# Kernel tuning notes

Measured on AMD Instinct MI355X. Metric: run time of the kernel, lower is better.

Reference implementation:

```python
import jax, jax.numpy as jnp
import numpy as np

B, S, F, D = 64, 129, 768, 4
MOM = 0.9
EPS = 1e-6


def setup_inputs() -> dict:
    key = jax.random.key(0)
    ks = jax.random.split(key, 8)
    x = jax.random.normal(ks[0], (B, S, F), dtype=jnp.float32)
    labels = jax.random.randint(ks[1], (B,), 0, 16, dtype=jnp.int32)
    domain = jax.random.randint(ks[2], (B,), 0, D, dtype=jnp.int32)
    lmda = jax.random.beta(ks[3], 0.1, 0.1, (B, 1, 1)).astype(jnp.float32)
    d_rand = jax.random.randint(ks[4], (B,), 1, D, dtype=jnp.int32)  # range(1, num_domains)
    mean_buf = (0.1 * jax.random.normal(ks[5], (D, F))).astype(jnp.float32)
    var_buf = jax.random.uniform(ks[6], (D, F), minval=0.5, maxval=1.5, dtype=jnp.float32)
    hg_noise = jax.random.normal(ks[7], (B, S, F), dtype=jnp.float32)
    return {"input": x, "lmda": lmda, "mean_buf": mean_buf, "var_buf": var_buf,
            "hg_noise": hg_noise, "labels": labels, "domain": domain, "d_rand": d_rand}


def reference(input, lmda, mean_buf, var_buf, hg_noise, labels, domain, d_rand):
    x = input  # [B,S,F]
    b, s, f = x.shape
    d = mean_buf.shape[0]

    # --- per-domain mean/var over dims [0,1] (unbiased), momentum buffer update ---
    tok = x.reshape(b * s, f)
    seg = jnp.repeat(domain, s)  # [B*S]
    cnt = jax.ops.segment_sum(jnp.ones((b * s,), x.dtype), seg, num_segments=d)  # tokens/domain
    s1 = jax.ops.segment_sum(tok, seg, num_segments=d)          # [D,F]
    s2 = jax.ops.segment_sum(tok * tok, seg, num_segments=d)    # [D,F]
    n = cnt[:, None]
    mu_d = s1 / jnp.maximum(n, 1.0)
    var_d = (s2 - n * mu_d * mu_d) / jnp.maximum(n - 1.0, 1.0)  # unbiased, matches torch.var
    present = (cnt > 0)[:, None]
    new_mean = jnp.where(present, MOM * mean_buf + (1.0 - MOM) * mu_d, mean_buf)
    new_var = jnp.where(present, MOM * var_buf + (1.0 - MOM) * var_d, var_buf)

    # --- instance renorm over token dim (unbiased var) + cross-domain restyle ---
    mu_i = x.mean(1, keepdims=True)
    v_i = x.var(1, keepdims=True, ddof=1)
    x_normed = (x - mu_i) * jax.lax.rsqrt(v_i + EPS)
    ds = (domain + d_rand) % d
    x_new = x_normed * jnp.sqrt(new_var[ds] + EPS)[:, None, :] + new_mean[ds][:, None, :]
    x_mix = lmda * x + (1.0 - lmda) * x_new

    # --- Gaussian hallucinated samples from own-domain stats ---
    hg = new_mean[domain][:, None, :] + jnp.sqrt(new_var[domain] + EPS)[:, None, :] * hg_noise

    # --- pairwise euclidean distance + hard example mining + soft-margin triplet loss ---
    xe = jnp.concatenate([x, x_mix, hg], axis=0).reshape(3 * b, s * f)  # [3B, S*F]
    ln = jnp.concatenate([labels, labels, -jnp.ones((b,), labels.dtype)])
    sq = jnp.sum(xe * xe, axis=1)
    d2 = sq[:, None] + sq[None, :] - 2.0 * (xe @ xe.T)
    dist = jnp.sqrt(jnp.clip(d2, 1e-12))
    pos = ln[:, None] == ln[None, :]
    big = jnp.asarray(1e30, dist.dtype)
    dist_ap = jnp.max(jnp.where(pos, dist, -big), axis=1)
    dist_an = jnp.min(jnp.where(pos, big, dist), axis=1)
    tri_hard_loss = jnp.mean(jax.nn.softplus(dist_ap - dist_an))  # SoftMarginLoss, y=1

    return x_mix, tri_hard_loss, new_mean, new_var
```

## Files before the change

### kernel.cpp

```cpp
#include <hip/hip_runtime.h>
#include <math.h>

#define B_ 64
#define S_ 129
#define F_ 768
#define N3 192
#define BF 49152
#define NCHUNK 1548
#define GMAIN 256
#define GSZ 36864
#define NSPLIT 8

#define WS_NM   0
#define WS_SV   3072
#define WS_C1   6144
#define WS_C0   55296
#define WS_HGM  104448
#define WS_HGS  153600
#define WS_S1   202752
#define WS_S2   251904
#define WS_GRAM 301056
#define WS_PART 337920
#define WS_S1P  WS_PART
#define WS_S2P  (WS_PART + NSPLIT * BF)

#define OUT_LOSS 6340608
#define OUT_NM   6340609
#define OUT_NV   6343681

typedef unsigned int uint;
using short8v = __attribute__((ext_vector_type(8))) short;
using float4v = __attribute__((ext_vector_type(4))) float;

__global__ void k_bf_stats(const float* __restrict__ x,
                           float* __restrict__ s1p, float* __restrict__ s2p) {
    int part = blockIdx.x / 48;
    int blk  = blockIdx.x % 48;
    int t4 = blk * 256 + threadIdx.x;
    int b = t4 / 192, f = (t4 - b * 192) * 4;
    int s0 = part * 16;
    int s1e = s0 + 16 + (part == 7 ? 1 : 0);
    const float* p = x + (size_t)b * S_ * F_ + f;
    float4 a1 = {0.f,0.f,0.f,0.f}, a2 = {0.f,0.f,0.f,0.f};
    for (int s = s0; s < s1e; ++s) {
        float4 v = *(const float4*)(p + s * F_);
        a1.x += v.x; a1.y += v.y; a1.z += v.z; a1.w += v.w;
        a2.x += v.x*v.x; a2.y += v.y*v.y; a2.z += v.z*v.z; a2.w += v.w*v.w;
    }
    *(float4*)(s1p + part * BF + b * F_ + f) = a1;
    *(float4*)(s2p + part * BF + b * F_ + f) = a2;
}

__global__ void k_sum(const float* __restrict__ s1p, const float* __restrict__ s2p,
                      float* __restrict__ s1, float* __restrict__ s2) {
    int j = (blockIdx.x * 256 + threadIdx.x) * 4;
    float4 a1 = {0.f,0.f,0.f,0.f}, a2 = {0.f,0.f,0.f,0.f};
#pragma unroll
    for (int p = 0; p < NSPLIT; ++p) {
        float4 v1 = *(const float4*)(s1p + p * BF + j);
        float4 v2 = *(const float4*)(s2p + p * BF + j);
        a1.x += v1.x; a1.y += v1.y; a1.z += v1.z; a1.w += v1.w;
        a2.x += v2.x; a2.y += v2.y; a2.z += v2.z; a2.w += v2.w;
    }
    *(float4*)(s1 + j) = a1;
    *(float4*)(s2 + j) = a2;
}

__global__ void k_dom(const float* __restrict__ s1, const float* __restrict__ s2,
                      const int* __restrict__ domain,
                      const float* __restrict__ mean_buf, const float* __restrict__ var_buf,
                      float* __restrict__ nm_tab, float* __restrict__ sv_tab,
                      float* __restrict__ out_nm, float* __restrict__ out_nv) {
    int idx = blockIdx.x * 256 + threadIdx.x;
    if (idx >= F_ * 4) return;
    int f = idx >> 2, d = idx & 3;
    float a1 = 0.f, a2 = 0.f, cntf = 0.f;
#pragma unroll 8
    for (int b = 0; b < B_; ++b) {
        float v1 = s1[b * F_ + f];
        float v2 = s2[b * F_ + f];
        bool mk = (domain[b] == d);
        a1 += mk ? v1 : 0.0f;
        a2 += mk ? v2 : 0.0f;
        cntf += mk ? 1.0f : 0.0f;
    }
    float nm, nv;
    if (cntf > 0.f) {
        float n = cntf * (float)S_;
        float mu = a1 / n;
        float var = (a2 - n * mu * mu) / fmaxf(n - 1.0f, 1.0f);
        nm = 0.9f * mean_buf[d * F_ + f] + 0.1f * mu;
        nv = 0.9f * var_buf[d * F_ + f] + 0.1f * var;
    } else {
        nm = mean_buf[d * F_ + f];
        nv = var_buf[d * F_ + f];
    }
    out_nm[d * F_ + f] = nm;
    out_nv[d * F_ + f] = nv;
    nm_tab[d * F_ + f] = nm;
    sv_tab[d * F_ + f] = sqrtf(nv + 1e-6f);
}

__global__ void k_coef(const float* __restrict__ s1, const float* __restrict__ s2,
                       const float* __restrict__ lmda,
                       const int* __restrict__ domain, const int* __restrict__ d_rand,
                       const float* __restrict__ nm_tab, const float* __restrict__ sv_tab,
                       float* __restrict__ c1, float* __restrict__ c0,
                       float* __restrict__ hgm, float* __restrict__ hgs,
                       float* __restrict__ gram, float* __restrict__ out_loss) {
    int t = blockIdx.x * 256 + threadIdx.x;
    if (blockIdx.x < 144) gram[blockIdx.x * 256 + threadIdx.x] = 0.0f;
    if (blockIdx.x == 144 && threadIdx.x == 0) out_loss[0] = 0.0f;
    int b = t / F_, f = t - b * F_;
    float mu = s1[t] * (1.0f / (float)S_);
    float v  = (s2[t] - (float)S_ * mu * mu) * (1.0f / (float)(S_ - 1));
    float r  = rsqrtf(v + 1e-6f);
    int dm = domain[b];
    int ds = (dm + d_rand[b]) & 3;
    float sv = sv_tab[ds * F_ + f];
    float nm = nm_tab[ds * F_ + f];
    float lam = lmda[b];
    float rs = r * sv;
    c1[t] = lam + (1.0f - lam) * rs;
    c0[t] = (1.0f - lam) * (nm - mu * rs);
    hgm[t] = nm_tab[dm * F_ + f];
    hgs[t] = sv_tab[dm * F_ + f];
}

__device__ __forceinline__ uint pack2(float a, float b) {
    uint ua = __float_as_uint(a);
    uint ub = __float_as_uint(b);
    uint ha = (ua + 0x7FFFu + ((ua >> 16) & 1u)) >> 16;
    uint hb = (ub + 0x7FFFu + ((ub >> 16) & 1u)) & 0xFFFF0000u;
    return hb | ha;
}

__device__ __forceinline__ void bf16_store8(char* lds, int row, int g,
                                            float4 v0, float4 v1) {
    uint4 H;
    H.x = pack2(v0.x, v0.y);
    H.y = pack2(v0.z, v0.w);
    H.z = pack2(v1.x, v1.y);
    H.w = pack2(v1.z, v1.w);
    *(uint4*)(lds + row * 128 + ((g ^ (row & 7)) << 4)) = H;
}

__device__ __forceinline__ float4 fma4(float4 a, float4 x, float4 b) {
    float4 r;
    r.x = fmaf(a.x, x.x, b.x); r.y = fmaf(a.y, x.y, b.y);
    r.z = fmaf(a.z, x.z, b.z); r.w = fmaf(a.w, x.w, b.w);
    return r;
}

template <bool EXCL>
__global__ __launch_bounds__(512, 2)
void k_main(const float* __restrict__ x, const float* __restrict__ hgn,
            const float* __restrict__ c1, const float* __restrict__ c0,
            const float* __restrict__ hgm, const float* __restrict__ hgs,
            float* __restrict__ xmix, float* part, int npart) {
    __shared__ __align__(16) char LDS[24576];
    float4v acc[6][3];
#pragma unroll
    for (int i = 0; i < 6; ++i)
#pragma unroll
        for (int j = 0; j < 3; ++j)
            acc[i][j] = (float4v){0.f, 0.f, 0.f, 0.f};

    int tid = threadIdx.x;
    int b = tid >> 3;
    int g = tid & 7;
    int w = tid >> 6;
    int wr = (w >> 2) * 96, wc = (w & 3) * 48;
    int lane = tid & 63, m = lane & 15, qd = lane >> 4;

    int q = blockIdx.x;
    size_t goff; int cb;
    {
        int s = q / 12, f0 = (q - s * 12) * 64;
        goff = ((size_t)b * S_ + s) * F_ + f0 + (g << 3);
        cb = b * F_ + f0 + (g << 3);
    }
    float4 X0 = ((const float4*)(x + goff))[0];
    float4 X1 = ((const float4*)(x + goff))[1];
    float4 N0 = ((const float4*)(hgn + goff))[0];
    float4 N1 = ((const float4*)(hgn + goff))[1];
    float4 C1a = ((const float4*)(c1 + cb))[0], C1b = ((const float4*)(c1 + cb))[1];
    float4 C0a = ((const float4*)(c0 + cb))[0], C0b = ((const float4*)(c0 + cb))[1];
    float4 HMa = ((const float4*)(hgm + cb))[0], HMb = ((const float4*)(hgm + cb))[1];
    float4 HSa = ((const float4*)(hgs + cb))[0], HSb = ((const float4*)(hgs + cb))[1];

    for (; q < NCHUNK; q += GMAIN) {
        float4 M0 = fma4(C1a, X0, C0a);
        float4 M1 = fma4(C1b, X1, C0b);
        ((float4*)(xmix + goff))[0] = M0;
        ((float4*)(xmix + goff))[1] = M1;
        float4 H0 = fma4(HSa, N0, HMa);
        float4 H1 = fma4(HSb, N1, HMb);

        bf16_store8(LDS, b, g, X0, X1);
        bf16_store8(LDS, 64 + b, g, M0, M1);
        bf16_store8(LDS, 128 + b, g, H0, H1);
        __syncthreads();

        int qn = q + GMAIN;
        if (qn < NCHUNK) {
            int s = qn / 12, f0 = (qn - s * 12) * 64;
            goff = ((size_t)b * S_ + s) * F_ + f0 + (g << 3);
            cb = b * F_ + f0 + (g << 3);
            X0 = ((const float4*)(x + goff))[0];
            X1 = ((const float4*)(x + goff))[1];
            N0 = ((const float4*)(hgn + goff))[0];
            N1 = ((const float4*)(hgn + goff))[1];
            C1a = ((const float4*)(c1 + cb))[0]; C1b = ((const float4*)(c1 + cb))[1];
            C0a = ((const float4*)(c0 + cb))[0]; C0b = ((const float4*)(c0 + cb))[1];
            HMa = ((const float4*)(hgm + cb))[0]; HMb = ((const float4*)(hgm + cb))[1];
            HSa = ((const float4*)(hgs + cb))[0]; HSb = ((const float4*)(hgs + cb))[1];
        }

#pragma unroll
        for (int t = 0; t < 2; ++t) {
            short8v A[6];
#pragma unroll
            for (int i = 0; i < 6; ++i) {
                int row = wr + i * 16 + m;
                int go = (((t << 2) + qd) ^ (row & 7)) << 4;
                A[i] = *(const short8v*)(LDS + row * 128 + go);
            }
#pragma unroll
            for (int j = 0; j < 3; ++j) {
                int row = wc + j * 16 + m;
                int go = (((t << 2) + qd) ^ (row & 7)) << 4;
                short8v Bv = *(const short8v*)(LDS + row * 128 + go);
#pragma unroll
                for (int i = 0; i < 6; ++i)
                    acc[i][j] = __builtin_amdgcn_mfma_f32_16x16x32_bf16(A[i], Bv, acc[i][j], 0, 0, 0);
            }
        }
        __syncthreads();
    }

    float* dst = part + (size_t)(blockIdx.x % npart) * GSZ;
#pragma unroll
    for (int i = 0; i < 6; ++i)
#pragma unroll
        for (int j = 0; j < 3; ++j) {
            int base = (wr + i * 16 + qd * 4) * N3 + wc + j * 16 + m;
#pragma unroll
            for (int r = 0; r < 4; ++r) {
                int o = base + r * N3;
                if (EXCL) dst[o] = acc[i][j][r];
                else atomicAdd(dst + o, acc[i][j][r]);
            }
        }
}

__global__ void k_red(const float* __restrict__ part, float* __restrict__ gram, int npart) {
    int g  = blockIdx.x / 36;
    int jb = blockIdx.x % 36;
    int j = (jb * 256 + threadIdx.x) * 4;
    int p0 = g * 32;
    int p1 = (p0 + 32 < npart) ? p0 + 32 : npart;
    float4 s = {0.f, 0.f, 0.f, 0.f};
    for (int p = p0; p < p1; ++p) {
        float4 v = *(const float4*)(part + (size_t)p * GSZ + j);
        s.x += v.x; s.y += v.y; s.z += v.z; s.w += v.w;
    }
    atomicAdd(gram + j,     s.x);
    atomicAdd(gram + j + 1, s.y);
    atomicAdd(gram + j + 2, s.z);
    atomicAdd(gram + j + 3, s.w);
}

__global__ void k_loss(const float* __restrict__ gram, const int* __restrict__ labels,
                       float* __restrict__ out_loss) {
    __shared__ float sq[N3];
    __shared__ int ln[N3];
    int i = blockIdx.x, lane = threadIdx.x;
    for (int k = lane; k < N3; k += 64) {
        sq[k] = gram[k * (N3 + 1)];
        ln[k] = (k < 128) ? labels[k & 63] : -1;
    }
    __syncthreads();
    int li = ln[i];
    float si = sq[i];
    float ap = -1e30f, an = 1e30f;
    for (int j = lane; j < N3; j += 64) {
        float d2 = si + sq[j] - 2.0f * gram[i * N3 + j];
        float dist = sqrtf(fmaxf(d2, 1e-12f));
        bool pos = (li == ln[j]);
        ap = pos ? fmaxf(ap, dist) : ap;
        an = pos ? an : fminf(an, dist);
    }
#pragma unroll
    for (int off = 32; off; off >>= 1) {
        ap = fmaxf(ap, __shfl_xor(ap, off));
        an = fminf(an, __shfl_xor(an, off));
    }
    if (lane == 0) {
        float xv = ap - an;
        float sp = fmaxf(xv, 0.0f) + log1pf(expf(-fabsf(xv)));
        atomicAdd(out_loss, sp * (1.0f / (float)N3));
    }
}

extern "C" void kernel_launch(void* const* d_in, const int* in_sizes, int n_in,
                              void* d_out, int out_size, void* d_ws, size_t ws_size,
                              hipStream_t stream) {
    const float* x        = (const float*)d_in[0];
    const float* lmda     = (const float*)d_in[1];
    const float* mean_buf = (const float*)d_in[2];
    const float* var_buf  = (const float*)d_in[3];
    const float* hgn      = (const float*)d_in[4];
    const int*   labels   = (const int*)d_in[5];
    const int*   domain   = (const int*)d_in[6];
    const int*   d_rand   = (const int*)d_in[7];
    float* out = (float*)d_out;
    float* ws  = (float*)d_ws;

    long avail = (long)(ws_size / 4) - WS_PART;
    int npart = (int)(avail / GSZ);
    if (npart < 1) npart = 1;
    if (npart > GMAIN) npart = GMAIN;
    bool excl = (npart == GMAIN);
    int ngroups = (npart + 31) / 32;

    k_bf_stats<<<dim3(48 * NSPLIT), dim3(256), 0, stream>>>(x, ws + WS_S1P, ws + WS_S2P);
    k_sum<<<dim3(48), dim3(256), 0, stream>>>(ws + WS_S1P, ws + WS_S2P,
                                              ws + WS_S1, ws + WS_S2);
    k_dom<<<dim3(12), dim3(256), 0, stream>>>(ws + WS_S1, ws + WS_S2, domain,
                                              mean_buf, var_buf,
                                              ws + WS_NM, ws + WS_SV,
                                              out + OUT_NM, out + OUT_NV);
    k_coef<<<dim3(192), dim3(256), 0, stream>>>(ws + WS_S1, ws + WS_S2, lmda,
                                                domain, d_rand,
                                                ws + WS_NM, ws + WS_SV,
                                                ws + WS_C1, ws + WS_C0,
                                                ws + WS_HGM, ws + WS_HGS,
                                                ws + WS_GRAM, out + OUT_LOSS);
    if (!excl) {
        hipMemsetAsync(ws + WS_PART, 0, (size_t)npart * GSZ * 4, stream);
    }
    if (excl) {
        k_main<true><<<dim3(GMAIN), dim3(512), 0, stream>>>(
            x, hgn, ws + WS_C1, ws + WS_C0, ws + WS_HGM, ws + WS_HGS,
            out, ws + WS_PART, npart);
    } else {
        k_main<false><<<dim3(GMAIN), dim3(512), 0, stream>>>(
            x, hgn, ws + WS_C1, ws + WS_C0, ws + WS_HGM, ws + WS_HGS,
            out, ws + WS_PART, npart);
    }
    k_red<<<dim3(ngroups * 36), dim3(256), 0, stream>>>(ws + WS_PART, ws + WS_GRAM, npart);
    k_loss<<<dim3(N3), dim3(64), 0, stream>>>(ws + WS_GRAM, labels, out + OUT_LOSS);
}
```

Baseline: 159.2 us.

## Double-buffer main Gram LDS, fuse stats reduction, replace atomic gram reduce

The main Gram kernel now alternates between two LDS buffers, which removes the trailing barrier in each chunk iteration at the cost of doubling shared memory per block. This may reduce occupancy under the 2-blocks launch bound. The per-sample stats pass is merged into a single kernel that reduces over the token dimension in LDS, dropping the separate partial-sum kernel and its global round trip. The partial Gram reduction becomes one non-atomic pass that writes the gram into a slot after the partials, so the gram zeroing in the coefficient kernel is removed and one fewer partial slot is available.

```diff
diff --git a/kernel.cpp b/kernel.cpp
--- a/kernel.cpp
+++ b/kernel.cpp
@@ -9,7 +9,6 @@
 #define NCHUNK 1548
 #define GMAIN 256
 #define GSZ 36864
-#define NSPLIT 8
 
 #define WS_NM   0
 #define WS_SV   3072
@@ -19,10 +18,7 @@
 #define WS_HGS  153600
 #define WS_S1   202752
 #define WS_S2   251904
-#define WS_GRAM 301056
 #define WS_PART 337920
-#define WS_S1P  WS_PART
-#define WS_S2P  (WS_PART + NSPLIT * BF)
 
 #define OUT_LOSS 6340608
 #define OUT_NM   6340609
@@ -32,38 +28,35 @@
 using short8v = __attribute__((ext_vector_type(8))) short;
 using float4v = __attribute__((ext_vector_type(4))) float;
 
-__global__ void k_bf_stats(const float* __restrict__ x,
-                           float* __restrict__ s1p, float* __restrict__ s2p) {
-    int part = blockIdx.x / 48;
-    int blk  = blockIdx.x % 48;
-    int t4 = blk * 256 + threadIdx.x;
-    int b = t4 / 192, f = (t4 - b * 192) * 4;
-    int s0 = part * 16;
-    int s1e = s0 + 16 + (part == 7 ? 1 : 0);
+__global__ void k_stats(const float* __restrict__ x,
+                        float* __restrict__ s1, float* __restrict__ s2) {
+    __shared__ float4 r1[256], r2[256];
+    int b = blockIdx.x / 3, fg = blockIdx.x % 3;
+    int c = threadIdx.x & 63, sp = threadIdx.x >> 6;
+    int f = fg * 256 + c * 4;
     const float* p = x + (size_t)b * S_ * F_ + f;
+    int s0 = sp * 32;
+    int se = s0 + 32 + (sp == 3 ? 1 : 0);
     float4 a1 = {0.f,0.f,0.f,0.f}, a2 = {0.f,0.f,0.f,0.f};
-    for (int s = s0; s < s1e; ++s) {
+#pragma unroll 4
+    for (int s = s0; s < se; ++s) {
         float4 v = *(const float4*)(p + s * F_);
         a1.x += v.x; a1.y += v.y; a1.z += v.z; a1.w += v.w;
         a2.x += v.x*v.x; a2.y += v.y*v.y; a2.z += v.z*v.z; a2.w += v.w*v.w;
     }
-    *(float4*)(s1p + part * BF + b * F_ + f) = a1;
-    *(float4*)(s2p + part * BF + b * F_ + f) = a2;
-}
-
-__global__ void k_sum(const float* __restrict__ s1p, const float* __restrict__ s2p,
-                      float* __restrict__ s1, float* __restrict__ s2) {
-    int j = (blockIdx.x * 256 + threadIdx.x) * 4;
-    float4 a1 = {0.f,0.f,0.f,0.f}, a2 = {0.f,0.f,0.f,0.f};
-#pragma unroll
-    for (int p = 0; p < NSPLIT; ++p) {
-        float4 v1 = *(const float4*)(s1p + p * BF + j);
-        float4 v2 = *(const float4*)(s2p + p * BF + j);
-        a1.x += v1.x; a1.y += v1.y; a1.z += v1.z; a1.w += v1.w;
-        a2.x += v2.x; a2.y += v2.y; a2.z += v2.z; a2.w += v2.w;
-    }
-    *(float4*)(s1 + j) = a1;
-    *(float4*)(s2 + j) = a2;
+    r1[threadIdx.x] = a1; r2[threadIdx.x] = a2;
+    __syncthreads();
+    if (sp == 0) {
+        float4 t1 = r1[c], t2 = r2[c];
+#pragma unroll
+        for (int k = 1; k < 4; ++k) {
+            float4 u1 = r1[k * 64 + c], u2 = r2[k * 64 + c];
+            t1.x += u1.x; t1.y += u1.y; t1.z += u1.z; t1.w += u1.w;
+            t2.x += u2.x; t2.y += u2.y; t2.z += u2.z; t2.w += u2.w;
+        }
+        *(float4*)(s1 + b * F_ + f) = t1;
+        *(float4*)(s2 + b * F_ + f) = t2;
+    }
 }
 
 __global__ void k_dom(const float* __restrict__ s1, const float* __restrict__ s2,
@@ -107,10 +100,9 @@
                        const float* __restrict__ nm_tab, const float* __restrict__ sv_tab,
                        float* __restrict__ c1, float* __restrict__ c0,
                        float* __restrict__ hgm, float* __restrict__ hgs,
-                       float* __restrict__ gram, float* __restrict__ out_loss) {
+                       float* __restrict__ out_loss) {
     int t = blockIdx.x * 256 + threadIdx.x;
-    if (blockIdx.x < 144) gram[blockIdx.x * 256 + threadIdx.x] = 0.0f;
-    if (blockIdx.x == 144 && threadIdx.x == 0) out_loss[0] = 0.0f;
+    if (blockIdx.x == 0 && threadIdx.x == 0) out_loss[0] = 0.0f;
     int b = t / F_, f = t - b * F_;
     float mu = s1[t] * (1.0f / (float)S_);
     float v  = (s2[t] - (float)S_ * mu * mu) * (1.0f / (float)(S_ - 1));
@@ -158,7 +150,7 @@
             const float* __restrict__ c1, const float* __restrict__ c0,
             const float* __restrict__ hgm, const float* __restrict__ hgs,
             float* __restrict__ xmix, float* part, int npart) {
-    __shared__ __align__(16) char LDS[24576];
+    __shared__ __align__(16) char LDS[49152];
     float4v acc[6][3];
 #pragma unroll
     for (int i = 0; i < 6; ++i)
@@ -189,7 +181,9 @@
     float4 HMa = ((const float4*)(hgm + cb))[0], HMb = ((const float4*)(hgm + cb))[1];
     float4 HSa = ((const float4*)(hgs + cb))[0], HSb = ((const float4*)(hgs + cb))[1];
 
+    int par = 0;
     for (; q < NCHUNK; q += GMAIN) {
+        char* buf = LDS + par * 24576;
         float4 M0 = fma4(C1a, X0, C0a);
         float4 M1 = fma4(C1b, X1, C0b);
         ((float4*)(xmix + goff))[0] = M0;
@@ -197,9 +191,9 @@
         float4 H0 = fma4(HSa, N0, HMa);
         float4 H1 = fma4(HSb, N1, HMb);
 
-        bf16_store8(LDS, b, g, X0, X1);
-        bf16_store8(LDS, 64 + b, g, M0, M1);
-        bf16_store8(LDS, 128 + b, g, H0, H1);
+        bf16_store8(buf, b, g, X0, X1);
+        bf16_store8(buf, 64 + b, g, M0, M1);
+        bf16_store8(buf, 128 + b, g, H0, H1);
         __syncthreads();
 
         int qn = q + GMAIN;
@@ -224,19 +218,19 @@
             for (int i = 0; i < 6; ++i) {
                 int row = wr + i * 16 + m;
                 int go = (((t << 2) + qd) ^ (row & 7)) << 4;
-                A[i] = *(const short8v*)(LDS + row * 128 + go);
+                A[i] = *(const short8v*)(buf + row * 128 + go);
             }
 #pragma unroll
             for (int j = 0; j < 3; ++j) {
                 int row = wc + j * 16 + m;
                 int go = (((t << 2) + qd) ^ (row & 7)) << 4;
-                short8v Bv = *(const short8v*)(LDS + row * 128 + go);
+                short8v Bv = *(const short8v*)(buf + row * 128 + go);
 #pragma unroll
                 for (int i = 0; i < 6; ++i)
                     acc[i][j] = __builtin_amdgcn_mfma_f32_16x16x32_bf16(A[i], Bv, acc[i][j], 0, 0, 0);
             }
         }
-        __syncthreads();
+        par ^= 1;
     }
 
     float* dst = part + (size_t)(blockIdx.x % npart) * GSZ;
@@ -255,20 +249,11 @@
 }
 
 __global__ void k_red(const float* __restrict__ part, float* __restrict__ gram, int npart) {
-    int g  = blockIdx.x / 36;
-    int jb = blockIdx.x % 36;
-    int j = (jb * 256 + threadIdx.x) * 4;
-    int p0 = g * 32;
-    int p1 = (p0 + 32 < npart) ? p0 + 32 : npart;
-    float4 s = {0.f, 0.f, 0.f, 0.f};
-    for (int p = p0; p < p1; ++p) {
-        float4 v = *(const float4*)(part + (size_t)p * GSZ + j);
-        s.x += v.x; s.y += v.y; s.z += v.z; s.w += v.w;
-    }
-    atomicAdd(gram + j,     s.x);
-    atomicAdd(gram + j + 1, s.y);
-    atomicAdd(gram + j + 2, s.z);
-    atomicAdd(gram + j + 3, s.w);
+    int j = blockIdx.x * 256 + threadIdx.x;
+    float s = 0.0f;
+#pragma unroll 8
+    for (int p = 0; p < npart; ++p) s += part[(size_t)p * GSZ + j];
+    gram[j] = s;
 }
 
 __global__ void k_loss(const float* __restrict__ gram, const int* __restrict__ labels,
@@ -318,15 +303,14 @@
     float* ws  = (float*)d_ws;
 
     long avail = (long)(ws_size / 4) - WS_PART;
-    int npart = (int)(avail / GSZ);
+    int npart = (int)(avail / GSZ) - 1;
     if (npart < 1) npart = 1;
     if (npart > GMAIN) npart = GMAIN;
     bool excl = (npart == GMAIN);
-    int ngroups = (npart + 31) / 32;
-
-    k_bf_stats<<<dim3(48 * NSPLIT), dim3(256), 0, stream>>>(x, ws + WS_S1P, ws + WS_S2P);
-    k_sum<<<dim3(48), dim3(256), 0, stream>>>(ws + WS_S1P, ws + WS_S2P,
-                                              ws + WS_S1, ws + WS_S2);
+    float* part = ws + WS_PART;
+    float* gram = ws + WS_PART + (size_t)npart * GSZ;
+
+    k_stats<<<dim3(192), dim3(256), 0, stream>>>(x, ws + WS_S1, ws + WS_S2);
     k_dom<<<dim3(12), dim3(256), 0, stream>>>(ws + WS_S1, ws + WS_S2, domain,
                                               mean_buf, var_buf,
                                               ws + WS_NM, ws + WS_SV,
@@ -336,19 +320,19 @@
                                                 ws + WS_NM, ws + WS_SV,
                                                 ws + WS_C1, ws + WS_C0,
                                                 ws + WS_HGM, ws + WS_HGS,
-                                                ws + WS_GRAM, out + OUT_LOSS);
+                                                out + OUT_LOSS);
     if (!excl) {
-        hipMemsetAsync(ws + WS_PART, 0, (size_t)npart * GSZ * 4, stream);
+        hipMemsetAsync(part, 0, (size_t)npart * GSZ * 4, stream);
     }
     if (excl) {
         k_main<true><<<dim3(GMAIN), dim3(512), 0, stream>>>(
             x, hgn, ws + WS_C1, ws + WS_C0, ws + WS_HGM, ws + WS_HGS,
-            out, ws + WS_PART, npart);
+            out, part, npart);
     } else {
         k_main<false><<<dim3(GMAIN), dim3(512), 0, stream>>>(
             x, hgn, ws + WS_C1, ws + WS_C0, ws + WS_HGM, ws + WS_HGS,
-            out, ws + WS_PART, npart);
-    }
-    k_red<<<dim3(ngroups * 36), dim3(256), 0, stream>>>(ws + WS_PART, ws + WS_GRAM, npart);
-    k_loss<<<dim3(N3), dim3(64), 0, stream>>>(ws + WS_GRAM, labels, out + OUT_LOSS);
-}
+            out, part, npart);
+    }
+    k_red<<<dim3(144), dim3(256), 0, stream>>>(part, gram, npart);
+    k_loss<<<dim3(N3), dim3(64), 0, stream>>>(gram, labels, out + OUT_LOSS);
+}
```

New measurement: 160.7 us. No clear change (+1.0%).
